# Optimization experiments

Measured on AMD Instinct MI355X. Metric: run time of the kernel, lower is better.

## Reference

```python
import jax, jax.numpy as jnp
import numpy as np

_SQRT1_2 = 0.7071067811865476

B, S, D, N, NCH = 4, 2048, 1024, 32768, 8


def setup_inputs() -> dict:
    key = jax.random.key(0)
    ks = jax.random.split(key, 6)
    return {
        "x": jax.random.normal(ks[0], (B, S, D), jnp.float32),
        "h": jax.random.normal(ks[1], (B, S, D), jnp.float32),
        "emb": jax.random.normal(ks[2], (N, D), jnp.float32),
        "tau_offset": jax.random.normal(ks[3], (B, S, 1), jnp.float32),
        "w_read": jax.random.normal(ks[4], (N, D), jnp.float32),
        "w_write": jax.random.normal(ks[5], (N, D), jnp.float32),
        "n_chunks": NCH,
    }


def _srw_chunked(x, h, emb_unit, tau_offset, w_read, w_write, n_chunks):
    b, s, d = x.shape
    n = emb_unit.shape[0]
    cs = n // n_chunks
    h_bf = h.astype(jnp.bfloat16)
    x_bf = x.astype(jnp.bfloat16)
    emb_bf = emb_unit.astype(jnp.bfloat16)
    read_bf = w_read.astype(jnp.bfloat16)
    write_bf = w_write.astype(jnp.bfloat16)
    z1 = jnp.zeros((b, s, 1), jnp.float32)

    # ---- pass 1: online score statistics over chunks of N ----
    @jax.checkpoint
    def stats_step(carry, i):
        s_sum, sq_sum, cube_sum, ns_sum, ns_sq = carry
        ec = jax.lax.dynamic_slice_in_dim(emb_bf, i * cs, cs, axis=0)
        sc = (h_bf @ ec.T).astype(jnp.float32)  # [B,S,cs]
        s_sum = s_sum + sc.sum(-1, keepdims=True)
        sq_sum = sq_sum + (sc ** 2).sum(-1, keepdims=True)
        cube_sum = cube_sum + (sc ** 3).sum(-1, keepdims=True)
        pns = sc.mean(axis=(0, 1))  # per-neuron mean score [cs]
        return ((s_sum, sq_sum, cube_sum, ns_sum + pns.sum(), ns_sq + (pns ** 2).sum()), None)

    (s_sum, sq_sum, cube_sum, ns_sum, ns_sq), _ = jax.lax.scan(
        stats_step, (z1, z1, z1, jnp.float32(0.0), jnp.float32(0.0)), jnp.arange(n_chunks))

    s_mean = s_sum / n
    s_std = jnp.sqrt(sq_sum / n - s_mean ** 2) + 1e-08
    tau = s_mean + tau_offset * s_std
    cube_mean = cube_sum / n
    central_third = cube_mean - 3.0 * s_mean * s_std ** 2 - s_mean ** 3
    score_skew = jax.lax.stop_gradient((central_third / (s_std ** 3 + 1e-08)).mean())
    mean_score = ns_sum / n
    var_score = ns_sq / n - mean_score ** 2
    score_lb = var_score / (mean_score ** 2 + var_score + 0.01)

    # ---- pass 2: erf-threshold gate + read/write GEMM accumulate ----
    @jax.checkpoint
    def gate_step(carry, i):
        out, wcost, gmax, act, strong, phib, zsum, z075c, z030c, glg = carry
        s0 = i * cs
        ec = jax.lax.dynamic_slice_in_dim(emb_bf, s0, cs, axis=0)
        rc = jax.lax.dynamic_slice_in_dim(read_bf, s0, cs, axis=0)
        wc = jax.lax.dynamic_slice_in_dim(write_bf, s0, cs, axis=0)
        rc = rc / (jnp.linalg.norm(rc, axis=-1, keepdims=True) + 1e-08)
        wc = wc / (jnp.linalg.norm(wc, axis=-1, keepdims=True) + 1e-08)
        z = ((h_bf @ ec.T).astype(jnp.float32) - tau) / s_std  # [B,S,cs]
        phi = 0.5 * (1.0 + jax.lax.erf(z * _SQRT1_2))
        gate = jnp.where(z > 0, z * phi, 0.0)
        xr = x_bf @ rc.T  # [B,S,cs]
        c_out = ((gate.astype(jnp.bfloat16) * xr) @ wc).astype(jnp.float32)  # [B,S,D]
        g_safe = gate + 1e-08
        new = (
            out + c_out,
            wcost + gate.sum(-1, keepdims=True),
            jnp.maximum(gmax, gate.max(-1, keepdims=True)),
            act + (gate > 0.0).astype(jnp.float32).sum(-1, keepdims=True),
            strong + (gate > 0.5).astype(jnp.float32).sum(-1, keepdims=True),
            phib + ((phi > 0.95) | (phi < 0.05)).astype(jnp.float32).sum(-1, keepdims=True),
            zsum + jnp.where(z > 0, z, 0.0).sum(-1, keepdims=True),
            z075c + ((z > 0) & (z < 0.75)).astype(jnp.float32).sum(-1, keepdims=True),
            z030c + ((z > 0) & (z < 0.3)).astype(jnp.float32).sum(-1, keepdims=True),
            glg + (gate * jnp.log(g_safe)).sum(-1, keepdims=True),
        )
        return (new, None)

    init = (jnp.zeros((b, s, d), jnp.float32), z1, jnp.full((b, s, 1), -1e9, jnp.float32),
            z1, z1, z1, z1, z1, z1, z1)
    (raw_out, wcost, gmax, act, strong, phib, zsum, z075c, z030c, glg), _ = jax.lax.scan(
        gate_step, init, jnp.arange(n_chunks))

    den = jnp.maximum(wcost, 1.0)
    out = (raw_out / den).astype(jnp.bfloat16)
    score_std_out = s_std.mean()
    es_out = wcost.mean()
    active_n_mean = act.mean()
    z_mean_active = zsum / (act + 1e-08)
    active_eps = act + 1e-08
    z_lt_075_frac = jax.lax.stop_gradient((z075c / active_eps).mean())
    z_lt_030_frac = jax.lax.stop_gradient((z030c / active_eps).mean())
    tau_abs_mean = jax.lax.stop_gradient(tau).mean()
    active_per_token_std = jax.lax.stop_gradient(act).std()
    gate_sum_eps = wcost + 1e-08
    entropy_per_token = -glg / gate_sum_eps + jnp.log(gate_sum_eps)
    gate_entropy = jax.lax.stop_gradient(entropy_per_token).mean()
    return (out.astype(jnp.float32), act / n, gmax, score_lb, score_std_out, es_out,
            active_n_mean, strong / n, phib / n, z_mean_active, tau_abs_mean,
            z_lt_075_frac, z_lt_030_frac, score_skew, active_per_token_std, gate_entropy)


def reference(x, h, emb, tau_offset, w_read, w_write, n_chunks):
    emb_unit = emb / (jnp.linalg.norm(emb, axis=-1, keepdims=True) + 1e-08)
    return _srw_chunked(x, h, emb_unit, tau_offset, w_read, w_write, n_chunks)
```

## Files before the change

kernel.cpp:

```cpp
#include <hip/hip_runtime.h>

#define DEV __device__ __forceinline__

typedef __attribute__((ext_vector_type(4))) float f32x4;
typedef __attribute__((ext_vector_type(8))) short s16x8;
typedef __attribute__((ext_vector_type(8))) unsigned short u16x8;

static const int NTOK = 8192;
static const int DD   = 1024;
static const int NNEU = 32768;
static const int NC   = 8192;

static const int OUT_ACT    = 8388608;
static const int OUT_GMAX   = 8396800;
static const int OUT_SLB    = 8404992;
static const int OUT_SSTD   = 8404993;
static const int OUT_ES     = 8404994;
static const int OUT_ANM    = 8404995;
static const int OUT_STRONG = 8404996;
static const int OUT_PHIB   = 8413188;
static const int OUT_ZMEAN  = 8421380;
static const int OUT_TAUM   = 8429572;
static const int OUT_Z75    = 8429573;
static const int OUT_Z30    = 8429574;
static const int OUT_SKEW   = 8429575;
static const int OUT_ASTD   = 8429576;
static const int OUT_ENT    = 8429577;

DEV unsigned short f2bf(float f){
  unsigned u = __float_as_uint(f);
  u += 0x7fffu + ((u >> 16) & 1u);
  return (unsigned short)(u >> 16);
}
DEV float bf2f(unsigned short h){ return __uint_as_float(((unsigned)h) << 16); }
DEV float rnd_bf(float f){ return bf2f(f2bf(f)); }

template<int AUX>
DEV void gl_lds16(const void* g, void* l){
  __builtin_amdgcn_global_load_lds(
      (const __attribute__((address_space(1))) unsigned int*)g,
      (__attribute__((address_space(3))) unsigned int*)l, 16, 0, AUX);
}

DEV f32x4 mfma16(s16x8 a, s16x8 b, f32x4 c){
  return __builtin_amdgcn_mfma_f32_16x16x32_bf16(a, b, c, 0, 0, 0);
}

template<int AUX>
DEV void stage4(const unsigned short* __restrict__ G, size_t ld, int k0,
                unsigned short* L, int t){
  #pragma unroll
  for (int i = 0; i < 4; i++){
    int ch = i*256 + t;
    int row = ch >> 3, c = ch & 7;
    int cs = c ^ (row & 7);
    int wb = (i*256 + (t & 192)) * 16;
    gl_lds16<AUX>(G + (size_t)row * ld + k0 + cs*8, (char*)L + wb);
  }
}

DEV s16x8 frg(const unsigned short* L, int R, int kk, int lq){
  int cc = ((kk >> 3) + lq) ^ (R & 7);
  return *(const s16x8*)((const char*)L + R*128 + cc*16);
}

DEV void waitv_bar(){
  asm volatile("s_waitcnt vmcnt(0)" ::: "memory");
  __builtin_amdgcn_s_barrier();
  __builtin_amdgcn_sched_barrier(0);
}

DEV int2 xcd64(){
  int orig = blockIdx.y * 64 + blockIdx.x;
  int xcd = orig & 7, p = orig >> 3;
  int sqy = p >> 6, off = p & 63;
  int2 r;
  r.x = xcd*8 + (off & 7);
  r.y = sqy*8 + (off >> 3);
  return r;
}


__global__ __launch_bounds__(256) void k_norms(const float* __restrict__ e,
    const float* __restrict__ r_, const float* __restrict__ w_,
    float* __restrict__ inv_e, float* __restrict__ inv_r, float* __restrict__ inv_w){
  int t = threadIdx.x, l = t & 63, wv = t >> 6;
  int row = blockIdx.x * 4 + wv;
  const float4* ep = (const float4*)(e  + (size_t)row * DD);
  const float4* rp = (const float4*)(r_ + (size_t)row * DD);
  const float4* wp = (const float4*)(w_ + (size_t)row * DD);
  float se = 0.f, sr = 0.f, sw = 0.f;
  #pragma unroll
  for (int j = 0; j < 4; j++){
    float4 v = ep[j*64 + l];
    se += v.x*v.x + v.y*v.y + v.z*v.z + v.w*v.w;
    float4 a = rp[j*64 + l];
    float a0 = rnd_bf(a.x), a1 = rnd_bf(a.y), a2 = rnd_bf(a.z), a3 = rnd_bf(a.w);
    sr += a0*a0 + a1*a1 + a2*a2 + a3*a3;
    float4 c = wp[j*64 + l];
    float c0 = rnd_bf(c.x), c1 = rnd_bf(c.y), c2 = rnd_bf(c.z), c3 = rnd_bf(c.w);
    sw += c0*c0 + c1*c1 + c2*c2 + c3*c3;
  }
  #pragma unroll
  for (int d = 1; d < 64; d <<= 1){
    se += __shfl_xor(se, d); sr += __shfl_xor(sr, d); sw += __shfl_xor(sw, d);
  }
  if (l == 0){
    inv_e[row] = 1.f / (sqrtf(se) + 1e-8f);
    inv_r[row] = 1.f / (sqrtf(sr) + 1e-8f);
    inv_w[row] = 1.f / (sqrtf(sw) + 1e-8f);
  }
}

__global__ __launch_bounds__(256) void k_cast_scale(const float* __restrict__ in,
    const float* __restrict__ inv, unsigned short* __restrict__ o, int round_first){
  size_t i = (size_t)blockIdx.x * 256 + threadIdx.x;
  int row = (int)(i >> 8);
  float s = inv[row];
  float4 v = ((const float4*)in)[i];
  ushort4 r;
  if (round_first){
    r.x = f2bf(rnd_bf(v.x) * s); r.y = f2bf(rnd_bf(v.y) * s);
    r.z = f2bf(rnd_bf(v.z) * s); r.w = f2bf(rnd_bf(v.w) * s);
  } else {
    r.x = f2bf(v.x * s); r.y = f2bf(v.y * s);
    r.z = f2bf(v.z * s); r.w = f2bf(v.w * s);
  }
  ((ushort4*)o)[i] = r;
}

__global__ __launch_bounds__(256) void k_cast(const float* __restrict__ in,
                                              unsigned short* __restrict__ o){
  size_t i = (size_t)blockIdx.x * 256 + threadIdx.x;
  float4 v = ((const float4*)in)[i];
  ushort4 r;
  r.x = f2bf(v.x); r.y = f2bf(v.y); r.z = f2bf(v.z); r.w = f2bf(v.w);
  ((ushort4*)o)[i] = r;
}

__global__ __launch_bounds__(256) void k_wcnT(const float* __restrict__ w_,
    const float* __restrict__ invw, unsigned short* __restrict__ o){
  __shared__ unsigned short tile[64][65];
  int t = threadIdx.x;
  int n0b = blockIdx.x * 64, d0 = blockIdx.y * 64;
  #pragma unroll
  for (int i = 0; i < 16; i++){
    int idx = t + i*256;
    int r = idx >> 6, c = idx & 63;
    float v = w_[(size_t)(n0b + r) * DD + d0 + c];
    tile[c][r] = f2bf(rnd_bf(v) * invw[n0b + r]);
  }
  __syncthreads();
  #pragma unroll
  for (int i = 0; i < 16; i++){
    int idx = t + i*256;
    int rd = idx >> 6, cn = idx & 63;
    o[(size_t)(d0 + rd) * NNEU + n0b + cn] = tile[rd][cn];
  }
}

__global__ __launch_bounds__(256) void k_hsum(const unsigned short* __restrict__ hb,
                                              float* __restrict__ hs){
  int t = threadIdx.x; int r0 = blockIdx.x * 128;
  float s[4] = {0.f, 0.f, 0.f, 0.f};
  for (int r = 0; r < 128; r++){
    const unsigned short* row = hb + (size_t)(r0 + r) * DD;
    #pragma unroll
    for (int j = 0; j < 4; j++) s[j] += bf2f(row[j*256 + t]);
  }
  #pragma unroll
  for (int j = 0; j < 4; j++) atomicAdd(hs + j*256 + t, s[j]);
}

__global__ __launch_bounds__(256) void k_pns(const unsigned short* __restrict__ eb,
    const float* __restrict__ hs, float* __restrict__ ns){
  __shared__ float hsh[1024];
  __shared__ float pr[8];
  int t = threadIdx.x, l = t & 63, wv = t >> 6;
  for (int i = t; i < 1024; i += 256) hsh[i] = hs[i];
  __syncthreads();
  float bs = 0.f, bq = 0.f;
  for (int it = 0; it < 32; it++){
    int row = blockIdx.x * 128 + it*4 + wv;
    const unsigned short* er = eb + (size_t)row * DD + l*16;
    float s = 0.f;
    #pragma unroll
    for (int j = 0; j < 16; j++) s += hsh[l*16 + j] * bf2f(er[j]);
    #pragma unroll
    for (int d = 1; d < 64; d <<= 1) s += __shfl_xor(s, d);
    float pns = s * (1.f / 8192.f);
    bs += pns; bq += pns * pns;
  }
  if (l == 0){ pr[wv*2] = bs; pr[wv*2 + 1] = bq; }
  __syncthreads();
  if (t == 0){
    atomicAdd(ns + 0, pr[0] + pr[2] + pr[4] + pr[6]);
    atomicAdd(ns + 1, pr[1] + pr[3] + pr[5] + pr[7]);
  }
}


template<bool DO_STATS>
__global__ __launch_bounds__(256, 2) void k_score(
    const unsigned short* __restrict__ A, const unsigned short* __restrict__ Bm,
    float* __restrict__ s_sum, float* __restrict__ sq_sum, float* __restrict__ cu_sum,
    unsigned short* __restrict__ Sout, int do_store)
{
  __shared__ unsigned short lds[32768];
  const int t = threadIdx.x, l = t & 63, wv = t >> 6;
  const int wm = wv >> 1, wn = wv & 1;
  const int lq = l >> 4, lr = l & 15;
  int2 rm = xcd64();
  const int bx = rm.x, by = rm.y;
  const unsigned short* Ab = A  + (size_t)by * 128 * DD;
  const unsigned short* Bb = Bm + (size_t)bx * 128 * DD;
  f32x4 acc[4][4];
  #pragma unroll
  for (int m = 0; m < 4; m++)
    #pragma unroll
    for (int n = 0; n < 4; n++) acc[m][n] = (f32x4){0.f, 0.f, 0.f, 0.f};

  stage4<0>(Ab, DD, 0, lds, t);
  stage4<0>(Bb, DD, 0, lds + 8192, t);
  waitv_bar();
  int cur = 0;
  for (int ks = 0; ks < 16; ++ks){
    unsigned short* Lc = lds + cur*16384;
    if (ks + 1 < 16){
      unsigned short* Ln = lds + (cur^1)*16384;
      int k0 = (ks+1)*64;
      stage4<0>(Ab, DD, k0, Ln, t);
      stage4<0>(Bb, DD, k0, Ln + 8192, t);
    }
    #pragma unroll
    for (int kk = 0; kk < 64; kk += 32){
      s16x8 af[4], bf4[4];
      #pragma unroll
      for (int m = 0; m < 4; m++) af[m]  = frg(Lc, wm*64 + m*16 + lr, kk, lq);
      #pragma unroll
      for (int n = 0; n < 4; n++) bf4[n] = frg(Lc + 8192, wn*64 + n*16 + lr, kk, lq);
      #pragma unroll
      for (int m = 0; m < 4; m++)
        #pragma unroll
        for (int n = 0; n < 4; n++)
          acc[m][n] = mfma16(af[m], bf4[n], acc[m][n]);
    }
    waitv_bar();
    cur ^= 1;
  }

  unsigned short* sl = lds;
  #pragma unroll
  for (int m = 0; m < 4; m++)
  #pragma unroll
  for (int n = 0; n < 4; n++)
  #pragma unroll
  for (int r = 0; r < 4; r++){
    int rl = wm*64 + m*16 + lq*4 + r;
    int cl = wn*64 + n*16 + lr;
    sl[rl*136 + cl] = f2bf(acc[m][n][r]);
  }
  __syncthreads();

  int row = t >> 1, half = t & 1;
  const unsigned short* sp = &sl[row*136 + half*64];
  unsigned short* Sdst = Sout + (size_t)(by*128 + row) * NC + bx*128 + half*64;
  float s1 = 0.f, s2 = 0.f, s3 = 0.f;
  #pragma unroll
  for (int j = 0; j < 8; j++){
    u16x8 v = *(const u16x8*)(sp + j*8);
    if (do_store) *(u16x8*)(Sdst + j*8) = v;
    if (DO_STATS){
      #pragma unroll
      for (int e = 0; e < 8; e++){
        float f = bf2f(v[e]);
        s1 += f; float f2 = f*f; s2 += f2; s3 += f2*f;
      }
    }
  }
  if (DO_STATS){
    s1 += __shfl_xor(s1, 1); s2 += __shfl_xor(s2, 1); s3 += __shfl_xor(s3, 1);
    if (half == 0){
      int gr = by*128 + row;
      atomicAdd(s_sum + gr, s1);
      atomicAdd(sq_sum + gr, s2);
      atomicAdd(cu_sum + gr, s3);
    }
  }
}

__global__ __launch_bounds__(256) void k_tau(const float* __restrict__ s_sum,
    const float* __restrict__ sq_sum, const float* __restrict__ tof,
    float* __restrict__ tau, float* __restrict__ rstd){
  int i = blockIdx.x * 256 + threadIdx.x;
  float mean = s_sum[i] * (1.f / 32768.f);
  float var  = sq_sum[i] * (1.f / 32768.f) - mean*mean;
  float sstd = sqrtf(fmaxf(var, 0.f)) + 1e-8f;
  tau[i]  = mean + tof[i] * sstd;
  rstd[i] = 1.f / sstd;
}


__global__ __launch_bounds__(256, 2) void k_gateS(
    const unsigned short* __restrict__ Xb, const unsigned short* __restrict__ Rb,
    const float* __restrict__ tau, const float* __restrict__ rstd,
    unsigned short* __restrict__ SP, int n0,
    float* __restrict__ wcostp, float* __restrict__ gmaxp, float* __restrict__ actp,
    float* __restrict__ strongp, float* __restrict__ phibp, float* __restrict__ zsump,
    float* __restrict__ z075p, float* __restrict__ z030p, float* __restrict__ glgp)
{
  __shared__ unsigned short lds[32768];
  const int t = threadIdx.x, l = t & 63, wv = t >> 6;
  const int wm = wv >> 1, wn = wv & 1;
  const int lq = l >> 4, lr = l & 15;
  int2 rm = xcd64();
  const int bx = rm.x, by = rm.y;
  const unsigned short* Xp = Xb + (size_t)by * 128 * DD;
  const unsigned short* Rp = Rb + (size_t)(n0 + bx*128) * DD;
  f32x4 accX[4][4];
  #pragma unroll
  for (int m = 0; m < 4; m++)
    #pragma unroll
    for (int n = 0; n < 4; n++) accX[m][n] = (f32x4){0.f,0.f,0.f,0.f};

  stage4<0>(Xp, DD, 0, lds, t);
  stage4<0>(Rp, DD, 0, lds + 8192, t);
  waitv_bar();
  int cur = 0;
  for (int ks = 0; ks < 16; ++ks){
    unsigned short* Lc = lds + cur*16384;
    if (ks + 1 < 16){
      unsigned short* Ln = lds + (cur^1)*16384;
      int k0 = (ks+1)*64;
      stage4<0>(Xp, DD, k0, Ln, t);
      stage4<0>(Rp, DD, k0, Ln + 8192, t);
    }
    #pragma unroll
    for (int kk = 0; kk < 64; kk += 32){
      s16x8 af[4], bf4[4];
      #pragma unroll
      for (int m = 0; m < 4; m++) af[m]  = frg(Lc, wm*64 + m*16 + lr, kk, lq);
      #pragma unroll
      for (int n = 0; n < 4; n++) bf4[n] = frg(Lc + 8192, wn*64 + n*16 + lr, kk, lq);
      #pragma unroll
      for (int m = 0; m < 4; m++)
        #pragma unroll
        for (int n = 0; n < 4; n++)
          accX[m][n] = mfma16(af[m], bf4[n], accX[m][n]);
    }
    waitv_bar();
    cur ^= 1;
  }

  unsigned short* plds = lds;
  #pragma unroll
  for (int m = 0; m < 4; m++)
  #pragma unroll
  for (int n = 0; n < 4; n++)
  #pragma unroll
  for (int r = 0; r < 4; r++){
    int rl = wm*64 + m*16 + lq*4 + r;
    int cl = wn*64 + n*16 + lr;
    plds[rl*136 + cl] = f2bf(accX[m][n][r]);
  }
  __syncthreads();

  int row = t >> 1, half = t & 1;
  int gr = by*128 + row;
  float tauv = tau[gr], rs = rstd[gr];
  unsigned short* Srow = SP + (size_t)gr * NC + bx*128 + half*64;
  const unsigned short* xrp = &plds[row*136 + half*64];
  float wsum = 0.f, gmx = 0.f, ac = 0.f, stc = 0.f, pb = 0.f;
  float zs = 0.f, z7 = 0.f, z3 = 0.f, gl = 0.f;
  #pragma unroll
  for (int j = 0; j < 8; j++){
    u16x8 sv8 = *(const u16x8*)(Srow + j*8);
    u16x8 pv;
    #pragma unroll
    for (int e = 0; e < 8; e++){
      float sc = bf2f(sv8[e]);
      float xr = bf2f(xrp[j*8 + e]);
      float z = (sc - tauv) * rs;
      float phi = 0.5f * (1.0f + erff(z * 0.70710678118654752440f));
      float gate = (z > 0.f) ? z * phi : 0.f;
      wsum += gate; gmx = fmaxf(gmx, gate);
      if (gate > 0.f)  ac  += 1.f;
      if (gate > 0.5f) stc += 1.f;
      if (phi > 0.95f || phi < 0.05f) pb += 1.f;
      if (z > 0.f){ zs += z; if (z < 0.75f) z7 += 1.f; if (z < 0.3f) z3 += 1.f; }
      gl += gate * __logf(gate + 1e-8f);
      pv[e] = f2bf(rnd_bf(gate) * xr);
    }
    *(u16x8*)(Srow + j*8) = pv;
  }
  wsum += __shfl_xor(wsum, 1); gmx = fmaxf(gmx, __shfl_xor(gmx, 1));
  ac   += __shfl_xor(ac, 1);   stc += __shfl_xor(stc, 1);
  pb   += __shfl_xor(pb, 1);   zs  += __shfl_xor(zs, 1);
  z7   += __shfl_xor(z7, 1);   z3  += __shfl_xor(z3, 1);
  gl   += __shfl_xor(gl, 1);
  if (half == 0){
    atomicAdd(wcostp + gr, wsum);
    atomicMax((int*)(gmaxp + gr), __float_as_int(gmx));
    atomicAdd(actp + gr, ac);
    atomicAdd(strongp + gr, stc);
    atomicAdd(phibp + gr, pb);
    atomicAdd(zsump + gr, zs);
    atomicAdd(z075p + gr, z7);
    atomicAdd(z030p + gr, z3);
    atomicAdd(glgp + gr, gl);
  }
}


__global__ __launch_bounds__(256, 2) void k_out_gemm(
    const unsigned short* __restrict__ Pm, const unsigned short* __restrict__ Bt,
    float* __restrict__ outp, const float* __restrict__ wcost, int accum, int fin)
{
  __shared__ unsigned short lds[32768];
  const int t = threadIdx.x, l = t & 63, wv = t >> 6;
  const int wm = wv >> 1, wn = wv & 1;
  const int lq = l >> 4, lr = l & 15;
  const int bx = blockIdx.x, by = blockIdx.y;
  const unsigned short* Ab = Pm + (size_t)by * 128 * NC;
  const unsigned short* Bb = Bt + (size_t)bx * 128 * NNEU;
  f32x4 acc[4][4];
  #pragma unroll
  for (int m = 0; m < 4; m++)
    #pragma unroll
    for (int n = 0; n < 4; n++) acc[m][n] = (f32x4){0.f,0.f,0.f,0.f};

  const int NT = NC / 64;
  stage4<2>(Ab, NC, 0, lds, t);
  stage4<0>(Bb, NNEU, 0, lds + 8192, t);
  waitv_bar();
  int cur = 0;
  for (int ks = 0; ks < NT; ++ks){
    unsigned short* Lc = lds + cur*16384;
    if (ks + 1 < NT){
      unsigned short* Ln = lds + (cur^1)*16384;
      int k0 = (ks+1)*64;
      stage4<2>(Ab, NC, k0, Ln, t);
      stage4<0>(Bb, NNEU, k0, Ln + 8192, t);
    }
    #pragma unroll
    for (int kk = 0; kk < 64; kk += 32){
      s16x8 af[4], bf4[4];
      #pragma unroll
      for (int m = 0; m < 4; m++) af[m]  = frg(Lc, wm*64 + m*16 + lr, kk, lq);
      #pragma unroll
      for (int n = 0; n < 4; n++) bf4[n] = frg(Lc + 8192, wn*64 + n*16 + lr, kk, lq);
      #pragma unroll
      for (int m = 0; m < 4; m++)
        #pragma unroll
        for (int n = 0; n < 4; n++)
          acc[m][n] = mfma16(af[m], bf4[n], acc[m][n]);
    }
    waitv_bar();
    cur ^= 1;
  }
  #pragma unroll
  for (int m = 0; m < 4; m++)
  #pragma unroll
  for (int r = 0; r < 4; r++){
    int gr = by*128 + wm*64 + m*16 + lq*4 + r;
    float den = fin ? fmaxf(wcost[gr], 1.f) : 1.f;
    #pragma unroll
    for (int n = 0; n < 4; n++){
      int dc = bx*128 + wn*64 + n*16 + lr;
      float* o = outp + (size_t)gr * DD + dc;
      float v = acc[m][n][r];
      if (accum) v += *o;
      if (fin)   v = rnd_bf(v / den);
      *o = v;
    }
  }
}


__global__ __launch_bounds__(1024) void k_final(
    const float* __restrict__ s_sum, const float* __restrict__ sq_sum,
    const float* __restrict__ cu_sum, const float* __restrict__ tof,
    const float* __restrict__ wcost, const float* __restrict__ gmax,
    const float* __restrict__ act, const float* __restrict__ strong,
    const float* __restrict__ phib, const float* __restrict__ zsum,
    const float* __restrict__ z075, const float* __restrict__ z030,
    const float* __restrict__ glg, const float* __restrict__ ns,
    float* __restrict__ out)
{
  int tid = threadIdx.x;
  float s0=0,s1=0,s2=0,s3=0,s4=0,s5=0,s6=0,s7=0,s8=0;
  for (int i = tid; i < NTOK; i += 1024){
    float mean = s_sum[i] * (1.f / 32768.f);
    float var  = sq_sum[i] * (1.f / 32768.f) - mean*mean;
    float sstd = sqrtf(fmaxf(var, 0.f)) + 1e-8f;
    float tauv = mean + tof[i] * sstd;
    float wc = wcost[i], ac = act[i];
    out[OUT_ACT + i]    = ac * (1.f / 32768.f);
    out[OUT_GMAX + i]   = gmax[i];
    out[OUT_STRONG + i] = strong[i] * (1.f / 32768.f);
    out[OUT_PHIB + i]   = phib[i] * (1.f / 32768.f);
    out[OUT_ZMEAN + i]  = zsum[i] / (ac + 1e-8f);
    float c3 = cu_sum[i] * (1.f / 32768.f) - 3.f*mean*sstd*sstd - mean*mean*mean;
    float skew = c3 / (sstd*sstd*sstd + 1e-8f);
    float gse = wc + 1e-8f;
    float ent = -glg[i] / gse + logf(gse);
    s0 += sstd; s1 += wc; s2 += ac; s3 += ac*ac; s4 += tauv;
    s5 += z075[i] / (ac + 1e-8f); s6 += z030[i] / (ac + 1e-8f); s7 += skew; s8 += ent;
  }
  __shared__ float rb[16][9];
  int lane = tid & 63, wid = tid >> 6;
  #pragma unroll
  for (int d = 1; d < 64; d <<= 1){
    s0 += __shfl_xor(s0,d); s1 += __shfl_xor(s1,d); s2 += __shfl_xor(s2,d);
    s3 += __shfl_xor(s3,d); s4 += __shfl_xor(s4,d); s5 += __shfl_xor(s5,d);
    s6 += __shfl_xor(s6,d); s7 += __shfl_xor(s7,d); s8 += __shfl_xor(s8,d);
  }
  if (lane == 0){
    rb[wid][0]=s0; rb[wid][1]=s1; rb[wid][2]=s2; rb[wid][3]=s3; rb[wid][4]=s4;
    rb[wid][5]=s5; rb[wid][6]=s6; rb[wid][7]=s7; rb[wid][8]=s8;
  }
  __syncthreads();
  if (tid == 0){
    float S[9];
    for (int k = 0; k < 9; k++){ float a = 0.f; for (int w2 = 0; w2 < 16; w2++) a += rb[w2][k]; S[k] = a; }
    const float inv = 1.f / 8192.f;
    float act_mean = S[2] * inv;
    out[OUT_SSTD] = S[0] * inv;
    out[OUT_ES]   = S[1] * inv;
    out[OUT_ANM]  = act_mean;
    out[OUT_ASTD] = sqrtf(fmaxf(S[3]*inv - act_mean*act_mean, 0.f));
    out[OUT_TAUM] = S[4] * inv;
    out[OUT_Z75]  = S[5] * inv;
    out[OUT_Z30]  = S[6] * inv;
    out[OUT_SKEW] = S[7] * inv;
    out[OUT_ENT]  = S[8] * inv;
    float ms = ns[0] * (1.f / 32768.f);
    float vs = ns[1] * (1.f / 32768.f) - ms*ms;
    out[OUT_SLB] = vs / (ms*ms + vs + 0.01f);
  }
}


extern "C" void kernel_launch(void* const* d_in, const int* in_sizes, int n_in,
                              void* d_out, int out_size, void* d_ws, size_t ws_size,
                              hipStream_t stream)
{
  (void)in_sizes; (void)n_in; (void)out_size;
  const float* x   = (const float*)d_in[0];
  const float* h   = (const float*)d_in[1];
  const float* emb = (const float*)d_in[2];
  const float* tof = (const float*)d_in[3];
  const float* wr  = (const float*)d_in[4];
  const float* ww  = (const float*)d_in[5];
  float* out = (float*)d_out;
  char* ws = (char*)d_ws;

  size_t off = 0;
  auto get = [&](size_t n){ size_t o = off; off += (n + 255) & ~(size_t)255; return o; };
  unsigned short* rcn_bf = (unsigned short*)(ws + get((size_t)NNEU*DD*2));
  unsigned short* emb_bf = (unsigned short*)(ws + get((size_t)NNEU*DD*2));
  unsigned short* wcnT   = (unsigned short*)(ws + get((size_t)DD*NNEU*2));
  unsigned short* h_bf   = (unsigned short*)(ws + get((size_t)NTOK*DD*2));
  unsigned short* x_bf   = (unsigned short*)(ws + get((size_t)NTOK*DD*2));
  float* inv_e = (float*)(ws + get(NNEU*4));
  float* inv_r = (float*)(ws + get(NNEU*4));
  float* inv_w = (float*)(ws + get(NNEU*4));
  size_t zoff = off;
  float* hsum   = (float*)(ws + get(DD*4));
  float* s_sum  = (float*)(ws + get(NTOK*4));
  float* sq_sum = (float*)(ws + get(NTOK*4));
  float* cu_sum = (float*)(ws + get(NTOK*4));
  float* tau    = (float*)(ws + get(NTOK*4));
  float* rstd   = (float*)(ws + get(NTOK*4));
  float* wcost  = (float*)(ws + get(NTOK*4));
  float* gmax   = (float*)(ws + get(NTOK*4));
  float* act    = (float*)(ws + get(NTOK*4));
  float* strong = (float*)(ws + get(NTOK*4));
  float* phib   = (float*)(ws + get(NTOK*4));
  float* zsum   = (float*)(ws + get(NTOK*4));
  float* z075   = (float*)(ws + get(NTOK*4));
  float* z030   = (float*)(ws + get(NTOK*4));
  float* glg    = (float*)(ws + get(NTOK*4));
  float* ns     = (float*)(ws + get(256));
  size_t zlen = off - zoff;

  const size_t szS = (size_t)NTOK * NC * 2;
  size_t poff = (off + 4095) & ~(size_t)4095;
  size_t avail = ws_size > poff ? ws_size - poff : 0;
  int kst = (int)(avail / szS);
  if (kst > 4) kst = 4;
  if (kst < 1) kst = 1;
  unsigned short* Sb = (unsigned short*)(ws + poff);

  hipMemsetAsync(ws + zoff, 0, zlen, stream);

  dim3 b256(256);
  dim3 gC(64, 64);
  k_norms<<<dim3(NNEU/4), b256, 0, stream>>>(emb, wr, ww, inv_e, inv_r, inv_w);
  k_cast_scale<<<dim3(NNEU*DD/4/256), b256, 0, stream>>>(emb, inv_e, emb_bf, 0);
  k_cast_scale<<<dim3(NNEU*DD/4/256), b256, 0, stream>>>(wr, inv_r, rcn_bf, 1);
  k_cast<<<dim3(NTOK*DD/4/256), b256, 0, stream>>>(h, h_bf);
  k_cast<<<dim3(NTOK*DD/4/256), b256, 0, stream>>>(x, x_bf);
  k_hsum<<<dim3(NTOK/128), b256, 0, stream>>>(h_bf, hsum);
  k_pns<<<dim3(NNEU/128), b256, 0, stream>>>(emb_bf, hsum, ns);

  for (int c = 0; c < 4; ++c){
    unsigned short* slot = Sb + (size_t)(c < kst ? c : 0) * NTOK * NC;
    k_score<true><<<gC, b256, 0, stream>>>(h_bf, emb_bf + (size_t)c*NC*DD,
        s_sum, sq_sum, cu_sum, slot, c < kst ? 1 : 0);
  }
  k_tau<<<dim3(NTOK/256), b256, 0, stream>>>(s_sum, sq_sum, tof, tau, rstd);
  k_wcnT<<<dim3(NNEU/64, DD/64), b256, 0, stream>>>(ww, inv_w, wcnT);

  for (int c = 0; c < 4; ++c){
    int slot_i = (c < kst) ? c : (c % kst);
    unsigned short* slot = Sb + (size_t)slot_i * NTOK * NC;
    if (c >= kst){
      k_score<false><<<gC, b256, 0, stream>>>(h_bf, emb_bf + (size_t)c*NC*DD,
          nullptr, nullptr, nullptr, slot, 1);
    }
    k_gateS<<<gC, b256, 0, stream>>>(x_bf, rcn_bf, tau, rstd, slot, c*NC,
        wcost, gmax, act, strong, phib, zsum, z075, z030, glg);
    k_out_gemm<<<dim3(DD/128, NTOK/128), b256, 0, stream>>>(slot, wcnT + (size_t)c*NC,
        out, wcost, c > 0 ? 1 : 0, c == 3 ? 1 : 0);
  }
  k_final<<<dim3(1), dim3(1024), 0, stream>>>(s_sum, sq_sum, cu_sum, tof, wcost, gmax,
      act, strong, phib, zsum, z075, z030, glg, ns, out);
}
```

Measured before the change: 3.777 ms.

## Fuse norm, cast and per-neuron mean; prefetch score tile into LDS in gate kernel

Replaces the separate norm, cast-scale and per-neuron-score kernels with one kernel per matrix. Each wave keeps its row in registers, normalizes it, writes bf16 and, for emb, computes the h-sum dot product in the same pass. This removes the extra fp32 reads of emb and w_read and the re-read of emb_bf. The gate kernel now loads its score tile into LDS asynchronously during the last K step, using a swizzled layout that matches the X·R tile, instead of reading it from global memory in the epilogue. This costs more LDS traffic and an extra swizzle, and the prefetch into the current buffer must not overlap data still in use.

```diff
diff --git a/kernel.cpp b/kernel.cpp
--- a/kernel.cpp
+++ b/kernel.cpp
@@ -59,6 +59,18 @@
   }
 }
 
+DEV void stageS(const unsigned short* __restrict__ S0, size_t ldS,
+                unsigned short* L, int t){
+  #pragma unroll
+  for (int i = 0; i < 8; i++){
+    int ch = i*256 + t;
+    int row = ch >> 4, c = ch & 15;
+    int cs = c ^ (row & 15);
+    int wb = (i*256 + (t & 192)) * 16;
+    gl_lds16<0>(S0 + (size_t)row * ldS + cs*8, (char*)L + wb);
+  }
+}
+
 DEV s16x8 frg(const unsigned short* L, int R, int kk, int lq){
   int cc = ((kk >> 3) + lq) ^ (R & 7);
   return *(const s16x8*)((const char*)L + R*128 + cc*16);
@@ -81,52 +93,75 @@
 }
 
 
-__global__ __launch_bounds__(256) void k_norms(const float* __restrict__ e,
-    const float* __restrict__ r_, const float* __restrict__ w_,
-    float* __restrict__ inv_e, float* __restrict__ inv_r, float* __restrict__ inv_w){
+template<int RND, int PNS>
+__global__ __launch_bounds__(256) void k_rncast(const float* __restrict__ in,
+    unsigned short* __restrict__ o, const float* __restrict__ hs,
+    float* __restrict__ ns){
+  __shared__ float hsh[1024];
+  __shared__ float pr[8];
+  int t = threadIdx.x, l = t & 63, wv = t >> 6;
+  if (PNS){
+    for (int i = t; i < 1024; i += 256) hsh[i] = hs[i];
+    __syncthreads();
+  }
+  int row = blockIdx.x * 4 + wv;
+  const float4* rp = (const float4*)(in + (size_t)row * DD);
+  float4 v[4];
+  float ss = 0.f;
+  #pragma unroll
+  for (int j = 0; j < 4; j++){
+    float4 a = rp[j*64 + l];
+    if (RND){ a.x = rnd_bf(a.x); a.y = rnd_bf(a.y); a.z = rnd_bf(a.z); a.w = rnd_bf(a.w); }
+    v[j] = a;
+    ss += a.x*a.x + a.y*a.y + a.z*a.z + a.w*a.w;
+  }
+  #pragma unroll
+  for (int d = 1; d < 64; d <<= 1) ss += __shfl_xor(ss, d);
+  float inv = 1.f / (sqrtf(ss) + 1e-8f);
+  float dot = 0.f;
+  ushort4* op = (ushort4*)(o + (size_t)row * DD);
+  #pragma unroll
+  for (int j = 0; j < 4; j++){
+    ushort4 r;
+    r.x = f2bf(v[j].x * inv); r.y = f2bf(v[j].y * inv);
+    r.z = f2bf(v[j].z * inv); r.w = f2bf(v[j].w * inv);
+    op[j*64 + l] = r;
+    if (PNS){
+      int c0 = (j*64 + l)*4;
+      dot += hsh[c0]*bf2f(r.x) + hsh[c0+1]*bf2f(r.y)
+           + hsh[c0+2]*bf2f(r.z) + hsh[c0+3]*bf2f(r.w);
+    }
+  }
+  if (PNS){
+    #pragma unroll
+    for (int d = 1; d < 64; d <<= 1) dot += __shfl_xor(dot, d);
+    if (l == 0){
+      float pns = dot * (1.f / 8192.f);
+      pr[wv*2] = pns; pr[wv*2 + 1] = pns*pns;
+    }
+    __syncthreads();
+    if (t == 0){
+      atomicAdd(ns + 0, pr[0] + pr[2] + pr[4] + pr[6]);
+      atomicAdd(ns + 1, pr[1] + pr[3] + pr[5] + pr[7]);
+    }
+  }
+}
+
+__global__ __launch_bounds__(256) void k_wnorm(const float* __restrict__ w_,
+                                               float* __restrict__ inv_w){
   int t = threadIdx.x, l = t & 63, wv = t >> 6;
   int row = blockIdx.x * 4 + wv;
-  const float4* ep = (const float4*)(e  + (size_t)row * DD);
-  const float4* rp = (const float4*)(r_ + (size_t)row * DD);
   const float4* wp = (const float4*)(w_ + (size_t)row * DD);
-  float se = 0.f, sr = 0.f, sw = 0.f;
+  float sw = 0.f;
   #pragma unroll
   for (int j = 0; j < 4; j++){
-    float4 v = ep[j*64 + l];
-    se += v.x*v.x + v.y*v.y + v.z*v.z + v.w*v.w;
-    float4 a = rp[j*64 + l];
-    float a0 = rnd_bf(a.x), a1 = rnd_bf(a.y), a2 = rnd_bf(a.z), a3 = rnd_bf(a.w);
-    sr += a0*a0 + a1*a1 + a2*a2 + a3*a3;
     float4 c = wp[j*64 + l];
     float c0 = rnd_bf(c.x), c1 = rnd_bf(c.y), c2 = rnd_bf(c.z), c3 = rnd_bf(c.w);
     sw += c0*c0 + c1*c1 + c2*c2 + c3*c3;
   }
   #pragma unroll
-  for (int d = 1; d < 64; d <<= 1){
-    se += __shfl_xor(se, d); sr += __shfl_xor(sr, d); sw += __shfl_xor(sw, d);
-  }
-  if (l == 0){
-    inv_e[row] = 1.f / (sqrtf(se) + 1e-8f);
-    inv_r[row] = 1.f / (sqrtf(sr) + 1e-8f);
-    inv_w[row] = 1.f / (sqrtf(sw) + 1e-8f);
-  }
-}
-
-__global__ __launch_bounds__(256) void k_cast_scale(const float* __restrict__ in,
-    const float* __restrict__ inv, unsigned short* __restrict__ o, int round_first){
-  size_t i = (size_t)blockIdx.x * 256 + threadIdx.x;
-  int row = (int)(i >> 8);
-  float s = inv[row];
-  float4 v = ((const float4*)in)[i];
-  ushort4 r;
-  if (round_first){
-    r.x = f2bf(rnd_bf(v.x) * s); r.y = f2bf(rnd_bf(v.y) * s);
-    r.z = f2bf(rnd_bf(v.z) * s); r.w = f2bf(rnd_bf(v.w) * s);
-  } else {
-    r.x = f2bf(v.x * s); r.y = f2bf(v.y * s);
-    r.z = f2bf(v.z * s); r.w = f2bf(v.w * s);
-  }
-  ((ushort4*)o)[i] = r;
+  for (int d = 1; d < 64; d <<= 1) sw += __shfl_xor(sw, d);
+  if (l == 0) inv_w[row] = 1.f / (sqrtf(sw) + 1e-8f);
 }
 
 __global__ __launch_bounds__(256) void k_cast(const float* __restrict__ in,
@@ -170,33 +205,6 @@
   }
   #pragma unroll
   for (int j = 0; j < 4; j++) atomicAdd(hs + j*256 + t, s[j]);
-}
-
-__global__ __launch_bounds__(256) void k_pns(const unsigned short* __restrict__ eb,
-    const float* __restrict__ hs, float* __restrict__ ns){
-  __shared__ float hsh[1024];
-  __shared__ float pr[8];
-  int t = threadIdx.x, l = t & 63, wv = t >> 6;
-  for (int i = t; i < 1024; i += 256) hsh[i] = hs[i];
-  __syncthreads();
-  float bs = 0.f, bq = 0.f;
-  for (int it = 0; it < 32; it++){
-    int row = blockIdx.x * 128 + it*4 + wv;
-    const unsigned short* er = eb + (size_t)row * DD + l*16;
-    float s = 0.f;
-    #pragma unroll
-    for (int j = 0; j < 16; j++) s += hsh[l*16 + j] * bf2f(er[j]);
-    #pragma unroll
-    for (int d = 1; d < 64; d <<= 1) s += __shfl_xor(s, d);
-    float pns = s * (1.f / 8192.f);
-    bs += pns; bq += pns * pns;
-  }
-  if (l == 0){ pr[wv*2] = bs; pr[wv*2 + 1] = bq; }
-  __syncthreads();
-  if (t == 0){
-    atomicAdd(ns + 0, pr[0] + pr[2] + pr[4] + pr[6]);
-    atomicAdd(ns + 1, pr[1] + pr[3] + pr[5] + pr[7]);
-  }
 }
 
 
@@ -317,6 +325,7 @@
   const int bx = rm.x, by = rm.y;
   const unsigned short* Xp = Xb + (size_t)by * 128 * DD;
   const unsigned short* Rp = Rb + (size_t)(n0 + bx*128) * DD;
+  const unsigned short* Stile = SP + (size_t)(by*128) * NC + bx*128;
   f32x4 accX[4][4];
   #pragma unroll
   for (int m = 0; m < 4; m++)
@@ -334,6 +343,8 @@
       int k0 = (ks+1)*64;
       stage4<0>(Xp, DD, k0, Ln, t);
       stage4<0>(Rp, DD, k0, Ln + 8192, t);
+    } else {
+      stageS(Stile, NC, lds, t);
     }
     #pragma unroll
     for (int kk = 0; kk < 64; kk += 32){
@@ -351,8 +362,7 @@
     waitv_bar();
     cur ^= 1;
   }
-
-  unsigned short* plds = lds;
+  unsigned short* xrl = lds + 16384;
   #pragma unroll
   for (int m = 0; m < 4; m++)
   #pragma unroll
@@ -361,25 +371,28 @@
   for (int r = 0; r < 4; r++){
     int rl = wm*64 + m*16 + lq*4 + r;
     int cl = wn*64 + n*16 + lr;
-    plds[rl*136 + cl] = f2bf(accX[m][n][r]);
+    int cs = (cl >> 3) ^ (rl & 15);
+    xrl[rl*128 + cs*8 + (cl & 7)] = f2bf(accX[m][n][r]);
   }
   __syncthreads();
 
   int row = t >> 1, half = t & 1;
   int gr = by*128 + row;
   float tauv = tau[gr], rs = rstd[gr];
-  unsigned short* Srow = SP + (size_t)gr * NC + bx*128 + half*64;
-  const unsigned short* xrp = &plds[row*136 + half*64];
+  unsigned short* Prow = SP + (size_t)gr * NC + bx*128 + half*64;
   float wsum = 0.f, gmx = 0.f, ac = 0.f, stc = 0.f, pb = 0.f;
   float zs = 0.f, z7 = 0.f, z3 = 0.f, gl = 0.f;
   #pragma unroll
-  for (int j = 0; j < 8; j++){
-    u16x8 sv8 = *(const u16x8*)(Srow + j*8);
+  for (int jj = 0; jj < 8; jj++){
+    int g  = half*8 + jj;
+    int cs = g ^ (row & 15);
+    u16x8 s8 = *(const u16x8*)&lds[row*128 + cs*8];
+    u16x8 x8 = *(const u16x8*)&lds[16384 + row*128 + cs*8];
     u16x8 pv;
     #pragma unroll
     for (int e = 0; e < 8; e++){
-      float sc = bf2f(sv8[e]);
-      float xr = bf2f(xrp[j*8 + e]);
+      float sc = bf2f(s8[e]);
+      float xr = bf2f(x8[e]);
       float z = (sc - tauv) * rs;
       float phi = 0.5f * (1.0f + erff(z * 0.70710678118654752440f));
       float gate = (z > 0.f) ? z * phi : 0.f;
@@ -391,7 +404,7 @@
       gl += gate * __logf(gate + 1e-8f);
       pv[e] = f2bf(rnd_bf(gate) * xr);
     }
-    *(u16x8*)(Srow + j*8) = pv;
+    *(u16x8*)(Prow + jj*8) = pv;
   }
   wsum += __shfl_xor(wsum, 1); gmx = fmaxf(gmx, __shfl_xor(gmx, 1));
   ac   += __shfl_xor(ac, 1);   stc += __shfl_xor(stc, 1);
@@ -562,8 +575,6 @@
   unsigned short* wcnT   = (unsigned short*)(ws + get((size_t)DD*NNEU*2));
   unsigned short* h_bf   = (unsigned short*)(ws + get((size_t)NTOK*DD*2));
   unsigned short* x_bf   = (unsigned short*)(ws + get((size_t)NTOK*DD*2));
-  float* inv_e = (float*)(ws + get(NNEU*4));
-  float* inv_r = (float*)(ws + get(NNEU*4));
   float* inv_w = (float*)(ws + get(NNEU*4));
   size_t zoff = off;
   float* hsum   = (float*)(ws + get(DD*4));
@@ -596,13 +607,12 @@
 
   dim3 b256(256);
   dim3 gC(64, 64);
-  k_norms<<<dim3(NNEU/4), b256, 0, stream>>>(emb, wr, ww, inv_e, inv_r, inv_w);
-  k_cast_scale<<<dim3(NNEU*DD/4/256), b256, 0, stream>>>(emb, inv_e, emb_bf, 0);
-  k_cast_scale<<<dim3(NNEU*DD/4/256), b256, 0, stream>>>(wr, inv_r, rcn_bf, 1);
   k_cast<<<dim3(NTOK*DD/4/256), b256, 0, stream>>>(h, h_bf);
   k_cast<<<dim3(NTOK*DD/4/256), b256, 0, stream>>>(x, x_bf);
   k_hsum<<<dim3(NTOK/128), b256, 0, stream>>>(h_bf, hsum);
-  k_pns<<<dim3(NNEU/128), b256, 0, stream>>>(emb_bf, hsum, ns);
+  k_rncast<0,1><<<dim3(NNEU/4), b256, 0, stream>>>(emb, emb_bf, hsum, ns);
+  k_rncast<1,0><<<dim3(NNEU/4), b256, 0, stream>>>(wr, rcn_bf, nullptr, nullptr);
+  k_wnorm<<<dim3(NNEU/4), b256, 0, stream>>>(ww, inv_w);
 
   for (int c = 0; c < 4; ++c){
     unsigned short* slot = Sb + (size_t)(c < kst ? c : 0) * NTOK * NC;
```

Result: slower. 3.859 ms (+2.2%).
